# Optimization experiments

Hardware: AMD Instinct MI355X
Metric: run time of the kernel (lower is better)

Reference implementation:

```python
import jax, jax.numpy as jnp
import numpy as np

B, T, C, H = 4096, 96, 256, 64  # batch, seq (<= BLOCK_SIZE=96), N_EMBED, head_size


def setup_inputs() -> dict:
    key = jax.random.key(0)
    k1, k2, k3, k4 = jax.random.split(key, 4)
    x = jax.random.normal(k1, (B, T, C), dtype=jnp.float32)
    # nn.Linear(C, H, bias=False) stores W as [H, C]; we keep [C, H] so y = x @ W.
    scale = 1.0 / jnp.sqrt(C)
    Wk = jax.random.normal(k2, (C, H), dtype=jnp.float32) * scale
    Wq = jax.random.normal(k3, (C, H), dtype=jnp.float32) * scale
    Wv = jax.random.normal(k4, (C, H), dtype=jnp.float32) * scale
    return {"x": x, "Wk": Wk, "Wq": Wq, "Wv": Wv}


def reference(x, Wk, Wq, Wv):
    Bx, Tx, Cx = x.shape
    k = x @ Wk                      # [B, T, H]
    q = x @ Wq                      # [B, T, H]
    v = x @ Wv                      # [B, T, H]
    # NOTE: original scales by C**-0.5 (embed dim), not head_size**-0.5.
    wei = jnp.einsum('bth,bsh->bts', q, k) * (Cx ** -0.5)  # [B, T, T]
    causal = jnp.tril(jnp.ones((Tx, Tx), dtype=bool))
    wei = jnp.where(causal, wei, -jnp.inf)
    wei = jax.nn.softmax(wei, axis=-1)
    # dropout is identity at eval time
    return jnp.einsum('bts,bsh->bth', wei, v)  # [B, T, H]
```

## Files before the change

kernel.cpp:

```cpp
#include <hip/hip_runtime.h>
#include <cstddef>


typedef __bf16 bf16x8 __attribute__((ext_vector_type(8)));
typedef float f32x4 __attribute__((ext_vector_type(4)));

static __device__ __forceinline__ unsigned short f2bf_u16(float f) {
  union { float f; unsigned int u; } c; c.f = f;
  return (unsigned short)((c.u + 0x7FFFu + ((c.u >> 16) & 1u)) >> 16);
}

__global__ void pack_w(const float* __restrict__ Wk, const float* __restrict__ Wq,
                       const float* __restrict__ Wv, unsigned short* __restrict__ pack) {
  int idx = blockIdx.x * blockDim.x + threadIdx.x;
  int lane = idx & 63;
  int t = idx >> 6;
  int nt = t & 3; t >>= 2;
  int kt = t & 7; t >>= 3;
  int p  = t;
  if (p >= 3) return;
  const float* W = (p == 0) ? Wk : (p == 1) ? Wq : Wv;
  int k0 = kt * 32 + (lane >> 4) * 8;
  int n  = nt * 16 + (lane & 15);
  unsigned short* dst = pack + (size_t)idx * 8;
#pragma unroll
  for (int j = 0; j < 8; ++j) dst[j] = f2bf_u16(W[(size_t)(k0 + j) * 64 + n]);
}

#define LDK 72
#define LDP 104
#define LDV 104

__global__ __launch_bounds__(768, 6) void head_fused(
    const float* __restrict__ x, const unsigned short* __restrict__ pack,
    float* __restrict__ out) {
  __shared__ __attribute__((aligned(16))) unsigned short ks2[2][96 * LDK];
  __shared__ __attribute__((aligned(16))) unsigned short SA [2][96 * LDP];
  __shared__ float rowsum[2][96];

  const int w    = threadIdx.x >> 6;
  const int half = w >= 6;
  const int w6   = w - 6 * half;
  const int lane = threadIdx.x & 63;
  const int lo   = lane & 15;
  const int hi   = lane >> 4;

  const int bb = 2 * blockIdx.x + half;
  const float* __restrict__ xb = x + (size_t)bb * (96 * 256);

  f32x4 acc[3][4];
#pragma unroll
  for (int p = 0; p < 3; ++p)
#pragma unroll
    for (int nt = 0; nt < 4; ++nt) acc[p][nt] = (f32x4){0.f, 0.f, 0.f, 0.f};

  const int am = 16 * w6 + lo;
#pragma unroll 2
  for (int kt = 0; kt < 8; ++kt) {
    const float* src = xb + (size_t)am * 256 + kt * 32 + hi * 8;
    f32x4 a0 = *(const f32x4*)src;
    f32x4 a1 = *(const f32x4*)(src + 4);
    union { bf16x8 v; unsigned short u[8]; } af;
#pragma unroll
    for (int j = 0; j < 4; ++j) { af.u[j] = f2bf_u16(a0[j]); af.u[4 + j] = f2bf_u16(a1[j]); }
#pragma unroll
    for (int p = 0; p < 3; ++p) {
#pragma unroll
      for (int nt = 0; nt < 4; ++nt) {
        bf16x8 bf = *(const bf16x8*)(pack + ((size_t)(((p * 8 + kt) * 4 + nt) * 64 + lane) * 8));
        acc[p][nt] = __builtin_amdgcn_mfma_f32_16x16x32_bf16(af.v, bf, acc[p][nt], 0, 0, 0);
      }
    }
  }

  unsigned short vv[16];
#pragma unroll
  for (int nt = 0; nt < 4; ++nt) {
#pragma unroll
    for (int r = 0; r < 4; ++r) {
      int row = 16 * w6 + hi * 4 + r;
      int col = 16 * nt + lo;
      ks2[half][row * LDK + col] = f2bf_u16(acc[0][nt][r]);
      SA [half][row * LDP + col] = f2bf_u16(acc[1][nt][r]);
      vv[nt * 4 + r] = f2bf_u16(acc[2][nt][r]);
    }
  }
  __syncthreads();

  f32x4 sacc[6];
#pragma unroll
  for (int jt = 0; jt < 6; ++jt) sacc[jt] = (f32x4){0.f, 0.f, 0.f, 0.f};

  bf16x8 qf0 = *(const bf16x8*)(SA[half] + (16 * w6 + lo) * LDP + hi * 8);
  bf16x8 qf1 = *(const bf16x8*)(SA[half] + (16 * w6 + lo) * LDP + 32 + hi * 8);
  for (int jt = 0; jt <= w6; ++jt) {
    bf16x8 kf0 = *(const bf16x8*)(ks2[half] + (16 * jt + lo) * LDK + hi * 8);
    bf16x8 kf1 = *(const bf16x8*)(ks2[half] + (16 * jt + lo) * LDK + 32 + hi * 8);
    sacc[jt] = __builtin_amdgcn_mfma_f32_16x16x32_bf16(qf0, kf0, sacc[jt], 0, 0, 0);
    sacc[jt] = __builtin_amdgcn_mfma_f32_16x16x32_bf16(qf1, kf1, sacc[jt], 0, 0, 0);
  }

#pragma unroll
  for (int r = 0; r < 4; ++r) {
    int row = 16 * w6 + hi * 4 + r;
    float pr[6];
    float mx = -1e30f;
    for (int jt = 0; jt <= w6; ++jt) {
      int col = 16 * jt + lo;
      float s = sacc[jt][r] * 0.0625f;
      s = (col <= row) ? s : -1e30f;
      pr[jt] = s;
      mx = fmaxf(mx, s);
    }
#pragma unroll
    for (int off = 1; off < 16; off <<= 1) mx = fmaxf(mx, __shfl_xor(mx, off, 64));
    float sum = 0.f;
    for (int jt = 0; jt <= w6; ++jt) {
      float p = __expf(pr[jt] - mx);
      pr[jt] = p;
      sum += p;
    }
#pragma unroll
    for (int off = 1; off < 16; off <<= 1) sum += __shfl_xor(sum, off, 64);
#pragma unroll
    for (int jt = 0; jt < 6; ++jt) {
      float p = (jt <= w6) ? pr[jt] : 0.f;
      SA[half][row * LDP + 16 * jt + lo] = f2bf_u16(p);
    }
    if (lo == 0) rowsum[half][row] = sum;
  }
  __syncthreads();

  unsigned short* vT = ks2[half];
#pragma unroll
  for (int nt = 0; nt < 4; ++nt) {
#pragma unroll
    for (int r = 0; r < 4; ++r) {
      int row = 16 * w6 + hi * 4 + r;
      int col = 16 * nt + lo;
      vT[col * LDV + row] = vv[nt * 4 + r];
    }
  }
  __syncthreads();

  f32x4 oacc[4];
#pragma unroll
  for (int nt = 0; nt < 4; ++nt) oacc[nt] = (f32x4){0.f, 0.f, 0.f, 0.f};

  const int ksmax = (16 * w6 + 15) >> 5;
  for (int ks = 0; ks <= ksmax; ++ks) {
    bf16x8 pf = *(const bf16x8*)(SA[half] + (16 * w6 + lo) * LDP + ks * 32 + hi * 8);
#pragma unroll
    for (int nt = 0; nt < 4; ++nt) {
      bf16x8 vf = *(const bf16x8*)(vT + (16 * nt + lo) * LDV + ks * 32 + hi * 8);
      oacc[nt] = __builtin_amdgcn_mfma_f32_16x16x32_bf16(pf, vf, oacc[nt], 0, 0, 0);
    }
  }

  float* __restrict__ ob = out + (size_t)bb * (96 * 64);
#pragma unroll
  for (int r = 0; r < 4; ++r) {
    int row = 16 * w6 + hi * 4 + r;
    float inv = 1.0f / rowsum[half][row];
#pragma unroll
    for (int nt = 0; nt < 4; ++nt) {
      ob[row * 64 + 16 * nt + lo] = oacc[nt][r] * inv;
    }
  }
}

extern "C" void kernel_launch(void* const* d_in, const int* in_sizes, int n_in,
                              void* d_out, int out_size, void* d_ws, size_t ws_size,
                              hipStream_t stream) {
  const float* x  = (const float*)d_in[0];
  const float* Wk = (const float*)d_in[1];
  const float* Wq = (const float*)d_in[2];
  const float* Wv = (const float*)d_in[3];
  float* out = (float*)d_out;
  unsigned short* pack = (unsigned short*)d_ws;

  const int B = in_sizes[0] / (96 * 256);

  pack_w<<<24, 256, 0, stream>>>(Wk, Wq, Wv, pack);
  head_fused<<<B / 2, 768, 0, stream>>>(x, pack, out);
}
```

Before: 692.9 us.

## Stage packed weights in LDS via async global-to-LDS double buffering

Rearranges the packed weight layout so each k-slice of all three projections is contiguous, then streams each slice into a double-buffered LDS region with global_load_lds, prefetching the next x fragment in registers. This replaces per-wave redundant global loads of the weights with one shared LDS copy per block and overlaps the next slice's loads with the current MFMAs. It adds a block-wide barrier on every k iteration and reuses the SA region as the staging buffer, and it raises register pressure from the prefetched x values.

```diff
diff --git a/kernel.cpp b/kernel.cpp
--- a/kernel.cpp
+++ b/kernel.cpp
@@ -4,6 +4,11 @@
 
 typedef __bf16 bf16x8 __attribute__((ext_vector_type(8)));
 typedef float f32x4 __attribute__((ext_vector_type(4)));
+
+#define GLOAD_LDS16(gp, lp)                                                     \
+  __builtin_amdgcn_global_load_lds(                                             \
+      (const __attribute__((address_space(1))) void*)(gp),                      \
+      (__attribute__((address_space(3))) void*)(lp), 16, 0, 0)
 
 static __device__ __forceinline__ unsigned short f2bf_u16(float f) {
   union { float f; unsigned int u; } c; c.f = f;
@@ -13,12 +18,12 @@
 __global__ void pack_w(const float* __restrict__ Wk, const float* __restrict__ Wq,
                        const float* __restrict__ Wv, unsigned short* __restrict__ pack) {
   int idx = blockIdx.x * blockDim.x + threadIdx.x;
+  if (idx >= 6144) return;
   int lane = idx & 63;
   int t = idx >> 6;
-  int nt = t & 3; t >>= 2;
-  int kt = t & 7; t >>= 3;
-  int p  = t;
-  if (p >= 3) return;
+  int nt = t & 3;
+  int p  = (t >> 2) % 3;
+  int kt = t / 12;
   const float* W = (p == 0) ? Wk : (p == 1) ? Wq : Wv;
   int k0 = kt * 32 + (lane >> 4) * 8;
   int n  = nt * 16 + (lane & 15);
@@ -34,9 +39,10 @@
 __global__ __launch_bounds__(768, 6) void head_fused(
     const float* __restrict__ x, const unsigned short* __restrict__ pack,
     float* __restrict__ out) {
-  __shared__ __attribute__((aligned(16))) unsigned short ks2[2][96 * LDK];
-  __shared__ __attribute__((aligned(16))) unsigned short SA [2][96 * LDP];
-  __shared__ float rowsum[2][96];
+  __shared__ __attribute__((aligned(16))) unsigned char smem[68352];
+  unsigned short* SA  = (unsigned short*)smem;
+  unsigned short* ks2 = (unsigned short*)(smem + 39936);
+  float*          rsm = (float*)(smem + 67584);
 
   const int w    = threadIdx.x >> 6;
   const int half = w >= 6;
@@ -48,6 +54,10 @@
   const int bb = 2 * blockIdx.x + half;
   const float* __restrict__ xb = x + (size_t)bb * (96 * 256);
 
+  unsigned short* SAh  = SA  + half * (96 * LDP);
+  unsigned short* ks2h = ks2 + half * (96 * LDK);
+  float*          rsh  = rsm + half * 96;
+
   f32x4 acc[3][4];
 #pragma unroll
   for (int p = 0; p < 3; ++p)
@@ -55,22 +65,37 @@
     for (int nt = 0; nt < 4; ++nt) acc[p][nt] = (f32x4){0.f, 0.f, 0.f, 0.f};
 
   const int am = 16 * w6 + lo;
-#pragma unroll 2
+  const float* xrow = xb + (size_t)am * 256 + hi * 8;
+
+  GLOAD_LDS16((const char*)pack + (size_t)threadIdx.x * 16,
+              smem + (size_t)w * 1024);
+  f32x4 a0 = *(const f32x4*)(xrow);
+  f32x4 a1 = *(const f32x4*)(xrow + 4);
+  __syncthreads();
+
   for (int kt = 0; kt < 8; ++kt) {
-    const float* src = xb + (size_t)am * 256 + kt * 32 + hi * 8;
-    f32x4 a0 = *(const f32x4*)src;
-    f32x4 a1 = *(const f32x4*)(src + 4);
+    const int cur = kt & 1;
+    f32x4 na0, na1;
+    if (kt < 7) {
+      GLOAD_LDS16((const char*)pack + (size_t)(kt + 1) * 12288 + (size_t)threadIdx.x * 16,
+                  smem + (size_t)(1 - cur) * 12288 + (size_t)w * 1024);
+      na0 = *(const f32x4*)(xrow + (kt + 1) * 32);
+      na1 = *(const f32x4*)(xrow + (kt + 1) * 32 + 4);
+    }
     union { bf16x8 v; unsigned short u[8]; } af;
 #pragma unroll
     for (int j = 0; j < 4; ++j) { af.u[j] = f2bf_u16(a0[j]); af.u[4 + j] = f2bf_u16(a1[j]); }
+    const unsigned short* pb = (const unsigned short*)(smem + cur * 12288);
 #pragma unroll
     for (int p = 0; p < 3; ++p) {
 #pragma unroll
       for (int nt = 0; nt < 4; ++nt) {
-        bf16x8 bf = *(const bf16x8*)(pack + ((size_t)(((p * 8 + kt) * 4 + nt) * 64 + lane) * 8));
+        bf16x8 bf = *(const bf16x8*)(pb + ((p * 4 + nt) * 64 + lane) * 8);
         acc[p][nt] = __builtin_amdgcn_mfma_f32_16x16x32_bf16(af.v, bf, acc[p][nt], 0, 0, 0);
       }
     }
+    if (kt < 7) { a0 = na0; a1 = na1; }
+    __syncthreads();
   }
 
   unsigned short vv[16];
@@ -80,8 +105,8 @@
     for (int r = 0; r < 4; ++r) {
       int row = 16 * w6 + hi * 4 + r;
       int col = 16 * nt + lo;
-      ks2[half][row * LDK + col] = f2bf_u16(acc[0][nt][r]);
-      SA [half][row * LDP + col] = f2bf_u16(acc[1][nt][r]);
+      ks2h[row * LDK + col] = f2bf_u16(acc[0][nt][r]);
+      SAh [row * LDP + col] = f2bf_u16(acc[1][nt][r]);
       vv[nt * 4 + r] = f2bf_u16(acc[2][nt][r]);
     }
   }
@@ -91,11 +116,11 @@
 #pragma unroll
   for (int jt = 0; jt < 6; ++jt) sacc[jt] = (f32x4){0.f, 0.f, 0.f, 0.f};
 
-  bf16x8 qf0 = *(const bf16x8*)(SA[half] + (16 * w6 + lo) * LDP + hi * 8);
-  bf16x8 qf1 = *(const bf16x8*)(SA[half] + (16 * w6 + lo) * LDP + 32 + hi * 8);
+  bf16x8 qf0 = *(const bf16x8*)(SAh + (16 * w6 + lo) * LDP + hi * 8);
+  bf16x8 qf1 = *(const bf16x8*)(SAh + (16 * w6 + lo) * LDP + 32 + hi * 8);
   for (int jt = 0; jt <= w6; ++jt) {
-    bf16x8 kf0 = *(const bf16x8*)(ks2[half] + (16 * jt + lo) * LDK + hi * 8);
-    bf16x8 kf1 = *(const bf16x8*)(ks2[half] + (16 * jt + lo) * LDK + 32 + hi * 8);
+    bf16x8 kf0 = *(const bf16x8*)(ks2h + (16 * jt + lo) * LDK + hi * 8);
+    bf16x8 kf1 = *(const bf16x8*)(ks2h + (16 * jt + lo) * LDK + 32 + hi * 8);
     sacc[jt] = __builtin_amdgcn_mfma_f32_16x16x32_bf16(qf0, kf0, sacc[jt], 0, 0, 0);
     sacc[jt] = __builtin_amdgcn_mfma_f32_16x16x32_bf16(qf1, kf1, sacc[jt], 0, 0, 0);
   }
@@ -125,13 +150,13 @@
 #pragma unroll
     for (int jt = 0; jt < 6; ++jt) {
       float p = (jt <= w6) ? pr[jt] : 0.f;
-      SA[half][row * LDP + 16 * jt + lo] = f2bf_u16(p);
-    }
-    if (lo == 0) rowsum[half][row] = sum;
-  }
-  __syncthreads();
-
-  unsigned short* vT = ks2[half];
+      SAh[row * LDP + 16 * jt + lo] = f2bf_u16(p);
+    }
+    if (lo == 0) rsh[row] = sum;
+  }
+  __syncthreads();
+
+  unsigned short* vT = ks2h;
 #pragma unroll
   for (int nt = 0; nt < 4; ++nt) {
 #pragma unroll
@@ -149,7 +174,7 @@
 
   const int ksmax = (16 * w6 + 15) >> 5;
   for (int ks = 0; ks <= ksmax; ++ks) {
-    bf16x8 pf = *(const bf16x8*)(SA[half] + (16 * w6 + lo) * LDP + ks * 32 + hi * 8);
+    bf16x8 pf = *(const bf16x8*)(SAh + (16 * w6 + lo) * LDP + ks * 32 + hi * 8);
 #pragma unroll
     for (int nt = 0; nt < 4; ++nt) {
       bf16x8 vf = *(const bf16x8*)(vT + (16 * nt + lo) * LDV + ks * 32 + hi * 8);
@@ -161,7 +186,7 @@
 #pragma unroll
   for (int r = 0; r < 4; ++r) {
     int row = 16 * w6 + hi * 4 + r;
-    float inv = 1.0f / rowsum[half][row];
+    float inv = 1.0f / rsh[row];
 #pragma unroll
     for (int nt = 0; nt < 4; ++nt) {
       ob[row * 64 + 16 * nt + lo] = oacc[nt][r] * inv;
```

Measured after the change: 659.7 us. 4.8% less time.
